# Optimization experiments

Hardware: AMD Instinct MI355X
Metric: run time of the kernel (lower is better)

## Reference

```python
import math
import jax, jax.numpy as jnp
import numpy as np

DIM_K = 64  # init arg: softmax scaling dimension


def setup_inputs() -> dict:
    k = jax.random.key(0)
    k1, k2, k3 = jax.random.split(k, 3)
    B, H, S, D = 4, 16, 4096, 64
    return {
        "query": jax.random.normal(k1, (B, H, S, D), dtype=jnp.float32),
        "key": jax.random.normal(k2, (B, H, S, D), dtype=jnp.float32),
        "value": jax.random.normal(k3, (B, H, S, D), dtype=jnp.float32),
        "causal_mask": 1,
    }


def reference(query, key, value, causal_mask):
    B, H, Q, dk = query.shape
    S = key.shape[2]
    dv = value.shape[-1]
    q = query / math.sqrt(DIM_K)
    chunk = max(1, min(int(math.sqrt(S)), S))
    n_chunks = S // chunk  # S chosen divisible by chunk
    neg_inf = jnp.float32(-jnp.inf)

    # [n_chunks, B, H, chunk, d]
    k_chunks = jnp.moveaxis(key.reshape(B, H, n_chunks, chunk, dk), 2, 0)
    v_chunks = jnp.moveaxis(value.reshape(B, H, n_chunks, chunk, dv), 2, 0)
    qpos = jnp.arange(Q)

    def step(carry, inputs):
        value_sum, normalizer, max_score = carry
        k_ch, v_ch, c_idx = inputs
        scores = jnp.einsum("bhqd,bhkd->bhqk", q, k_ch)  # [B,H,Q,chunk]
        if causal_mask:
            kpos = c_idx * chunk + jnp.arange(chunk)
            mask = qpos[:, None] >= kpos[None, :]
            scores = jnp.where(mask[None, None], scores, neg_inf)
        max_prev = max_score
        max_score = jnp.maximum(max_score, scores.max(axis=-1))
        exp_chunk = jnp.exp(scores - max_score[..., None])
        exp_prev = jnp.exp(max_prev - max_score)
        value_sum = value_sum * exp_prev[..., None] + jnp.einsum(
            "bhqk,bhkd->bhqd", exp_chunk, v_ch
        )
        normalizer = normalizer * exp_prev + exp_chunk.sum(axis=-1)
        return (value_sum, normalizer, max_score), None

    init = (
        jnp.zeros((B, H, Q, dv), dtype=query.dtype),
        jnp.zeros((B, H, Q), dtype=query.dtype),
        jnp.full((B, H, Q), neg_inf, dtype=query.dtype),
    )
    (value_sum, normalizer, _), _ = jax.lax.scan(
        step, init, (k_chunks, v_chunks, jnp.arange(n_chunks))
    )
    return value_sum / normalizer[..., None]
```

## Files before the change

kernel.cpp:

```cpp
#include <hip/hip_runtime.h>
#include <hip/hip_bf16.h>

typedef __attribute__((ext_vector_type(8))) __bf16 bf16x8;
typedef __attribute__((ext_vector_type(4))) float floatx4;

#define S_LEN 4096
#define NBH   64
#define BM    256
#define NW    8
#define BN    64
#define KSTR  72
#define C_SCALE 0.18033688011112042f

__device__ __forceinline__ short f2bf(float x) {
  __hip_bfloat16 h = __float2bfloat16(x);
  return *reinterpret_cast<const short*>(&h);
}

__global__ __launch_bounds__(512)
void mea_fwd(const float* __restrict__ qp, const float* __restrict__ kp,
             const float* __restrict__ vp, const int* __restrict__ cm,
             float* __restrict__ op)
{
  __shared__ short kL[BN * KSTR];
  __shared__ short vT[64 * KSTR];

  const int t    = threadIdx.x;
  const int w    = t >> 6;
  const int lane = t & 63;
  const int lg   = lane >> 4;
  const int l16  = lane & 15;

  const int bh  = blockIdx.y;
  const int qt  = (int)(gridDim.x - 1) - (int)blockIdx.x;
  const int q0  = qt * BM;
  const int qw0 = q0 + w * 32;
  const long base = (long)bh * S_LEN * 64;
  const int causal = cm[0];

  const int skr = t >> 3;
  const int sd0 = (t & 7) * 8;
  const int pcol = ((skr >> 4) & 1) * 32 + ((skr >> 3) & 1) * 16 +
                   ((skr >> 2) & 1) * 8  + ((skr >> 5) & 1) * 4 + (skr & 3);
  const int svcol = (pcol + (sd0 >> 4) * 16) & 63;

  bf16x8 qfrag[2][2];
#pragma unroll
  for (int nt = 0; nt < 2; ++nt)
#pragma unroll
    for (int ks = 0; ks < 2; ++ks) {
      const float* qr = qp + base + (long)(qw0 + nt*16 + l16) * 64 + ks*32 + lg*8;
      float4 a = *(const float4*)(qr);
      float4 b = *(const float4*)(qr + 4);
      union { short s[8]; bf16x8 v; } u;
      u.s[0]=f2bf(a.x*C_SCALE); u.s[1]=f2bf(a.y*C_SCALE);
      u.s[2]=f2bf(a.z*C_SCALE); u.s[3]=f2bf(a.w*C_SCALE);
      u.s[4]=f2bf(b.x*C_SCALE); u.s[5]=f2bf(b.y*C_SCALE);
      u.s[6]=f2bf(b.z*C_SCALE); u.s[7]=f2bf(b.w*C_SCALE);
      qfrag[nt][ks] = u.v;
    }

  floatx4 oacc[2][4];
#pragma unroll
  for (int i = 0; i < 2; ++i)
#pragma unroll
    for (int j = 0; j < 4; ++j)
      oacc[i][j] = (floatx4){0.f, 0.f, 0.f, 0.f};

  float m_run[2] = {-__builtin_inff(), -__builtin_inff()};
  float l_run[2] = {0.f, 0.f};

  const int kmax   = causal ? (q0 + BM) : S_LEN;
  const int ntiles = kmax / BN;

  float4 kpre[2], vpre[2];
  {
    const float* kb = kp + base + (long)skr * 64 + sd0;
    kpre[0] = ((const float4*)kb)[0];
    kpre[1] = ((const float4*)kb)[1];
    const float* vb = vp + base + (long)skr * 64 + sd0;
    vpre[0] = ((const float4*)vb)[0];
    vpre[1] = ((const float4*)vb)[1];
  }

  for (int kt = 0; kt < ntiles; ++kt) {
    const int k0 = kt * BN;

    {
      union { short s[8]; uint4 u; } pk;
      pk.s[0]=f2bf(kpre[0].x); pk.s[1]=f2bf(kpre[0].y);
      pk.s[2]=f2bf(kpre[0].z); pk.s[3]=f2bf(kpre[0].w);
      pk.s[4]=f2bf(kpre[1].x); pk.s[5]=f2bf(kpre[1].y);
      pk.s[6]=f2bf(kpre[1].z); pk.s[7]=f2bf(kpre[1].w);
      *(uint4*)(&kL[skr * KSTR + sd0]) = pk.u;

      short vs[8];
      vs[0]=f2bf(vpre[0].x); vs[1]=f2bf(vpre[0].y);
      vs[2]=f2bf(vpre[0].z); vs[3]=f2bf(vpre[0].w);
      vs[4]=f2bf(vpre[1].x); vs[5]=f2bf(vpre[1].y);
      vs[6]=f2bf(vpre[1].z); vs[7]=f2bf(vpre[1].w);
#pragma unroll
      for (int i = 0; i < 8; ++i)
        vT[(sd0 + i) * KSTR + svcol] = vs[i];
    }
    __syncthreads();

    if (kt + 1 < ntiles) {
      const int kn = k0 + BN;
      const float* kb = kp + base + (long)(kn + skr) * 64 + sd0;
      kpre[0] = ((const float4*)kb)[0];
      kpre[1] = ((const float4*)kb)[1];
      const float* vb = vp + base + (long)(kn + skr) * 64 + sd0;
      vpre[0] = ((const float4*)vb)[0];
      vpre[1] = ((const float4*)vb)[1];
    }

    if (!(causal && k0 >= qw0 + 32)) {
      floatx4 sacc[4][2];
#pragma unroll
      for (int mt = 0; mt < 4; ++mt)
#pragma unroll
        for (int nt = 0; nt < 2; ++nt)
          sacc[mt][nt] = (floatx4){0.f, 0.f, 0.f, 0.f};
#pragma unroll
      for (int ks = 0; ks < 2; ++ks)
#pragma unroll
        for (int mt = 0; mt < 4; ++mt) {
          bf16x8 kfrag = *(const bf16x8*)(&kL[(mt*16 + l16) * KSTR + ks*32 + lg*8]);
#pragma unroll
          for (int nt = 0; nt < 2; ++nt)
            sacc[mt][nt] = __builtin_amdgcn_mfma_f32_16x16x32_bf16(kfrag, qfrag[nt][ks], sacc[mt][nt], 0, 0, 0);
        }

      const bool needmask = causal && (k0 + BN - 1 > qw0);
      float mnew[2] = {m_run[0], m_run[1]};
#pragma unroll
      for (int mt = 0; mt < 4; ++mt)
#pragma unroll
        for (int nt = 0; nt < 2; ++nt)
#pragma unroll
          for (int r = 0; r < 4; ++r) {
            float v = sacc[mt][nt][r];
            if (needmask) {
              int key = k0  + mt*16 + lg*4 + r;
              int q   = qw0 + nt*16 + l16;
              if (q < key) v = -__builtin_inff();
            }
            sacc[mt][nt][r] = v;
            mnew[nt] = fmaxf(mnew[nt], v);
          }
#pragma unroll
      for (int nt = 0; nt < 2; ++nt) {
        mnew[nt] = fmaxf(mnew[nt], __shfl_xor(mnew[nt], 16));
        mnew[nt] = fmaxf(mnew[nt], __shfl_xor(mnew[nt], 32));
      }
      float alpha[2], rsum[2];
#pragma unroll
      for (int nt = 0; nt < 2; ++nt) {
        alpha[nt] = __builtin_amdgcn_exp2f(m_run[nt] - mnew[nt]);
        m_run[nt] = mnew[nt];
        rsum[nt]  = 0.f;
      }
      bf16x8 pfrag[2][2];
#pragma unroll
      for (int nt = 0; nt < 2; ++nt)
#pragma unroll
        for (int ks = 0; ks < 2; ++ks) {
          union { short s[8]; bf16x8 v; } pk;
#pragma unroll
          for (int r = 0; r < 4; ++r) {
            float e0 = __builtin_amdgcn_exp2f(sacc[ks][nt][r]     - mnew[nt]);
            float e1 = __builtin_amdgcn_exp2f(sacc[ks + 2][nt][r] - mnew[nt]);
            rsum[nt] += e0 + e1;
            pk.s[r]     = f2bf(e0);
            pk.s[4 + r] = f2bf(e1);
          }
          pfrag[nt][ks] = pk.v;
        }
#pragma unroll
      for (int nt = 0; nt < 2; ++nt) {
        rsum[nt] += __shfl_xor(rsum[nt], 16);
        rsum[nt] += __shfl_xor(rsum[nt], 32);
        l_run[nt] = l_run[nt] * alpha[nt] + rsum[nt];
      }
#pragma unroll
      for (int mo = 0; mo < 2; ++mo)
#pragma unroll
        for (int r = 0; r < 4; ++r) {
          float al = __shfl(alpha[mo], lg*4 + r);
#pragma unroll
          for (int nd = 0; nd < 4; ++nd)
            oacc[mo][nd][r] *= al;
        }

#pragma unroll
      for (int ks = 0; ks < 2; ++ks) {
        bf16x8 vfrag[4];
#pragma unroll
        for (int nd = 0; nd < 4; ++nd) {
          int colr = (ks*32 + lg*8 + nd*16) & 63;
          vfrag[nd] = *(const bf16x8*)(&vT[(nd*16 + l16) * KSTR + colr]);
        }
#pragma unroll
        for (int mo = 0; mo < 2; ++mo)
#pragma unroll
          for (int nd = 0; nd < 4; ++nd)
            oacc[mo][nd] = __builtin_amdgcn_mfma_f32_16x16x32_bf16(pfrag[mo][ks], vfrag[nd], oacc[mo][nd], 0, 0, 0);
      }
    }

    __syncthreads();
  }

#pragma unroll
  for (int mo = 0; mo < 2; ++mo)
#pragma unroll
    for (int r = 0; r < 4; ++r) {
      float lv  = __shfl(l_run[mo], lg*4 + r);
      float inv = __builtin_amdgcn_rcpf(lv);
      int qrow  = qw0 + mo*16 + lg*4 + r;
#pragma unroll
      for (int nd = 0; nd < 4; ++nd)
        op[base + (long)qrow * 64 + nd*16 + l16] = oacc[mo][nd][r] * inv;
    }
}

extern "C" void kernel_launch(void* const* d_in, const int* in_sizes, int n_in,
                              void* d_out, int out_size, void* d_ws, size_t ws_size,
                              hipStream_t stream) {
  const float* q = (const float*)d_in[0];
  const float* k = (const float*)d_in[1];
  const float* v = (const float*)d_in[2];
  const int*  cm = (const int*)d_in[3];
  float* o = (float*)d_out;
  dim3 grid(S_LEN / BM, NBH);
  mea_fwd<<<grid, dim3(512, 1, 1), 0, stream>>>(q, k, v, cm, o);
}
```

Before: 645.7 us.

## Double-buffer K/V shared tiles and process 128-key phases per barrier

Loads 128 keys per phase, two 64-key sub-tiles, into double-buffered shared memory. This halves the number of barriers and removes the trailing __syncthreads, since the next phase writes to the other buffer. Register prefetch doubles to cover two sub-tiles, and launch bounds now request 4 waves per EU. The trade-off is more LDS per block and higher register pressure from the larger prefetch.

```diff
diff --git a/kernel.cpp b/kernel.cpp
--- a/kernel.cpp
+++ b/kernel.cpp
@@ -7,9 +7,10 @@
 #define S_LEN 4096
 #define NBH   64
 #define BM    256
-#define NW    8
 #define BN    64
+#define PH    128
 #define KSTR  72
+#define VSTR  136
 #define C_SCALE 0.18033688011112042f
 
 __device__ __forceinline__ short f2bf(float x) {
@@ -17,13 +18,13 @@
   return *reinterpret_cast<const short*>(&h);
 }
 
-__global__ __launch_bounds__(512)
+__global__ __launch_bounds__(512, 4)
 void mea_fwd(const float* __restrict__ qp, const float* __restrict__ kp,
              const float* __restrict__ vp, const int* __restrict__ cm,
              float* __restrict__ op)
 {
-  __shared__ short kL[BN * KSTR];
-  __shared__ short vT[64 * KSTR];
+  __shared__ short kL[2][PH * KSTR];
+  __shared__ short vT[2][64 * VSTR];
 
   const int t    = threadIdx.x;
   const int w    = t >> 6;
@@ -70,52 +71,60 @@
   float m_run[2] = {-__builtin_inff(), -__builtin_inff()};
   float l_run[2] = {0.f, 0.f};
 
-  const int kmax   = causal ? (q0 + BM) : S_LEN;
-  const int ntiles = kmax / BN;
-
-  float4 kpre[2], vpre[2];
+  const int kmax = causal ? (q0 + BM) : S_LEN;
+  const int nph  = kmax / PH;
+
+  float4 kpre[2][2], vpre[2][2];
   {
     const float* kb = kp + base + (long)skr * 64 + sd0;
-    kpre[0] = ((const float4*)kb)[0];
-    kpre[1] = ((const float4*)kb)[1];
+    kpre[0][0] = ((const float4*)kb)[0];        kpre[0][1] = ((const float4*)kb)[1];
+    kpre[1][0] = ((const float4*)(kb + 4096))[0]; kpre[1][1] = ((const float4*)(kb + 4096))[1];
     const float* vb = vp + base + (long)skr * 64 + sd0;
-    vpre[0] = ((const float4*)vb)[0];
-    vpre[1] = ((const float4*)vb)[1];
+    vpre[0][0] = ((const float4*)vb)[0];        vpre[0][1] = ((const float4*)vb)[1];
+    vpre[1][0] = ((const float4*)(vb + 4096))[0]; vpre[1][1] = ((const float4*)(vb + 4096))[1];
   }
 
-  for (int kt = 0; kt < ntiles; ++kt) {
-    const int k0 = kt * BN;
-
-    {
+  int cur = 0;
+  for (int ph = 0; ph < nph; ++ph) {
+
+#pragma unroll
+    for (int h = 0; h < 2; ++h) {
       union { short s[8]; uint4 u; } pk;
-      pk.s[0]=f2bf(kpre[0].x); pk.s[1]=f2bf(kpre[0].y);
-      pk.s[2]=f2bf(kpre[0].z); pk.s[3]=f2bf(kpre[0].w);
-      pk.s[4]=f2bf(kpre[1].x); pk.s[5]=f2bf(kpre[1].y);
-      pk.s[6]=f2bf(kpre[1].z); pk.s[7]=f2bf(kpre[1].w);
-      *(uint4*)(&kL[skr * KSTR + sd0]) = pk.u;
+      pk.s[0]=f2bf(kpre[h][0].x); pk.s[1]=f2bf(kpre[h][0].y);
+      pk.s[2]=f2bf(kpre[h][0].z); pk.s[3]=f2bf(kpre[h][0].w);
+      pk.s[4]=f2bf(kpre[h][1].x); pk.s[5]=f2bf(kpre[h][1].y);
+      pk.s[6]=f2bf(kpre[h][1].z); pk.s[7]=f2bf(kpre[h][1].w);
+      *(uint4*)(&kL[cur][(h*64 + skr) * KSTR + sd0]) = pk.u;
 
       short vs[8];
-      vs[0]=f2bf(vpre[0].x); vs[1]=f2bf(vpre[0].y);
-      vs[2]=f2bf(vpre[0].z); vs[3]=f2bf(vpre[0].w);
-      vs[4]=f2bf(vpre[1].x); vs[5]=f2bf(vpre[1].y);
-      vs[6]=f2bf(vpre[1].z); vs[7]=f2bf(vpre[1].w);
+      vs[0]=f2bf(vpre[h][0].x); vs[1]=f2bf(vpre[h][0].y);
+      vs[2]=f2bf(vpre[h][0].z); vs[3]=f2bf(vpre[h][0].w);
+      vs[4]=f2bf(vpre[h][1].x); vs[5]=f2bf(vpre[h][1].y);
+      vs[6]=f2bf(vpre[h][1].z); vs[7]=f2bf(vpre[h][1].w);
 #pragma unroll
       for (int i = 0; i < 8; ++i)
-        vT[(sd0 + i) * KSTR + svcol] = vs[i];
+        vT[cur][(sd0 + i) * VSTR + h*64 + svcol] = vs[i];
     }
     __syncthreads();
 
-    if (kt + 1 < ntiles) {
-      const int kn = k0 + BN;
+    if (ph + 1 < nph) {
+      const int kn = (ph + 1) * PH;
       const float* kb = kp + base + (long)(kn + skr) * 64 + sd0;
-      kpre[0] = ((const float4*)kb)[0];
-      kpre[1] = ((const float4*)kb)[1];
+      kpre[0][0] = ((const float4*)kb)[0];        kpre[0][1] = ((const float4*)kb)[1];
+      kpre[1][0] = ((const float4*)(kb + 4096))[0]; kpre[1][1] = ((const float4*)(kb + 4096))[1];
       const float* vb = vp + base + (long)(kn + skr) * 64 + sd0;
-      vpre[0] = ((const float4*)vb)[0];
-      vpre[1] = ((const float4*)vb)[1];
-    }
-
-    if (!(causal && k0 >= qw0 + 32)) {
+      vpre[0][0] = ((const float4*)vb)[0];        vpre[0][1] = ((const float4*)vb)[1];
+      vpre[1][0] = ((const float4*)(vb + 4096))[0]; vpre[1][1] = ((const float4*)(vb + 4096))[1];
+    }
+
+    const short* kb_ = kL[cur];
+    const short* vb_ = vT[cur];
+
+#pragma unroll
+    for (int sub = 0; sub < 2; ++sub) {
+      const int k0 = ph * PH + sub * 64;
+      if (causal && k0 >= qw0 + 32) continue;
+
       floatx4 sacc[4][2];
 #pragma unroll
       for (int mt = 0; mt < 4; ++mt)
@@ -126,7 +135,7 @@
       for (int ks = 0; ks < 2; ++ks)
 #pragma unroll
         for (int mt = 0; mt < 4; ++mt) {
-          bf16x8 kfrag = *(const bf16x8*)(&kL[(mt*16 + l16) * KSTR + ks*32 + lg*8]);
+          bf16x8 kfrag = *(const bf16x8*)(&kb_[(sub*64 + mt*16 + l16) * KSTR + ks*32 + lg*8]);
 #pragma unroll
           for (int nt = 0; nt < 2; ++nt)
             sacc[mt][nt] = __builtin_amdgcn_mfma_f32_16x16x32_bf16(kfrag, qfrag[nt][ks], sacc[mt][nt], 0, 0, 0);
@@ -199,7 +208,7 @@
 #pragma unroll
         for (int nd = 0; nd < 4; ++nd) {
           int colr = (ks*32 + lg*8 + nd*16) & 63;
-          vfrag[nd] = *(const bf16x8*)(&vT[(nd*16 + l16) * KSTR + colr]);
+          vfrag[nd] = *(const bf16x8*)(&vb_[(nd*16 + l16) * VSTR + sub*64 + colr]);
         }
 #pragma unroll
         for (int mo = 0; mo < 2; ++mo)
@@ -209,7 +218,7 @@
       }
     }
 
-    __syncthreads();
+    cur ^= 1;
   }
 
 #pragma unroll
```

Measured after the change: 901.7 us. 1.4x slower.
